# Kernel tuning notes

Hardware: AMD Instinct MI355X
Metric: run time of the kernel (lower is better)

The kernel has to match this reference:

```python
import jax, jax.numpy as jnp
import numpy as np

CLUSTER_DIM = 64
SHRINKAGE = True
EPS = 1e-8


def setup_inputs() -> dict:
    key = jax.random.key(0)
    x = jax.random.normal(key, (256, CLUSTER_DIM, 4096), dtype=jnp.float32)
    return {"x": x}


def _mat_shrinkage(C, n):
    # Rao-Blackwellized Ledoit-Wolf shrinkage toward scaled identity.
    p = CLUSTER_DIM
    I = jnp.eye(p, dtype=C.dtype)[None, :, :]
    trace = jnp.trace(C, axis1=-2, axis2=-1)[:, None, None]          # [B,1,1]
    F_hat = trace / p * I
    second_trace = jnp.einsum('bij,bji->b', C, C)[:, None, None]      # tr(C @ C)
    numerator = (n - 2) / n * second_trace + trace ** 2
    denominator = (n + 2) * (second_trace - trace ** 2 / p)
    rho = jnp.minimum(numerator / denominator, 1.0)
    return rho * F_hat + (1.0 - rho) * C


def reference(x):
    B, C, M = x.shape  # C == CLUSTER_DIM
    x_mu = jnp.mean(x, axis=2, keepdims=True)
    x_cnt = x - x_mu                                                  # [B,C,M]
    cov = jnp.einsum('bcm,bdm->bcd', x_cnt, x_cnt) / M                # [B,C,C]
    if SHRINKAGE:
        cov = _mat_shrinkage(cov, n=M)
    L, Q = jnp.linalg.eigh(cov)                                       # L:[B,C] Q:[B,C,C]
    L = jnp.maximum(L, EPS)
    # S_hat = Q @ diag(L^-1/2) @ Q^T, fused as scaled columns of Q
    S_hat = jnp.einsum('bik,bk,bjk->bij', Q, jax.lax.rsqrt(L), Q)     # [B,C,C]
    Z = jnp.einsum('bij,bjm->bim', S_hat, x_cnt)                      # [B,C,M]
    return Z
```

## Files before the change

kernel.cpp:

```cpp
#include <hip/hip_runtime.h>
#include <hip/hip_bf16.h>

#define BB 256
#define P 64
#define MM 4096
#define MC 128
#define MT 256

using bf16x8 = __attribute__((ext_vector_type(8))) short;
using f32x16 = __attribute__((ext_vector_type(16))) float;
using f32x4  = __attribute__((ext_vector_type(4))) float;
using u32x4  = __attribute__((ext_vector_type(4))) unsigned;
using u32x2  = __attribute__((ext_vector_type(2))) unsigned;

__device__ inline f32x16 MF(bf16x8 a, bf16x8 b, f32x16 c) {
    return __builtin_amdgcn_mfma_f32_32x32x16_bf16(a, b, c, 0, 0, 0);
}
__device__ inline unsigned cvtpk(float lo, float hi) {
    unsigned u;
    asm("v_cvt_pk_bf16_f32 %0, %1, %2" : "=v"(u) : "v"(lo), "v"(hi));
    return u;
}

template<bool XPK>
__global__ __launch_bounds__(256)
void covpart_kernel(const float* __restrict__ x, float* __restrict__ s2p,
                    float* __restrict__ s1p, unsigned* __restrict__ xpk, int nsplit)
{
    __shared__ __align__(16) unsigned char smem[34816];

    const int b = blockIdx.x, sp = blockIdx.y;
    const int t = threadIdx.x;
    const int w = t >> 6, l = t & 63;
    const int lr = l & 31, lh = l >> 5;
    const int mlen = MM / nsplit;
    const float* xb = x + (size_t)b * (P * MM) + (size_t)sp * mlen;
    unsigned* xpb = XPK ? (xpk + (size_t)b * (32 * MM) + (size_t)sp * mlen) : nullptr;

    f32x16 acc0 = {0,0,0,0,0,0,0,0,0,0,0,0,0,0,0,0};
    f32x16 acc1 = {0,0,0,0,0,0,0,0,0,0,0,0,0,0,0,0};
    f32x16 acc2 = {0,0,0,0,0,0,0,0,0,0,0,0,0,0,0,0};
    f32x16 accse = {0,0,0,0,0,0,0,0,0,0,0,0,0,0,0,0};
    f32x16 accso = {0,0,0,0,0,0,0,0,0,0,0,0,0,0,0,0};
    const bf16x8 ones = {0x3F80,0x3F80,0x3F80,0x3F80,0x3F80,0x3F80,0x3F80,0x3F80};

    const int kbase = lh * 16;
    const int nch = mlen / MC;

    f32x4 ve[4], vo[4];
    #pragma unroll
    for (int j = 0; j < 4; ++j) {
        int slot = t + 256 * j;
        int dp = slot >> 5, c = (slot & 31) << 2;
        const float* p = xb + (size_t)(2 * dp) * MM + c;
        ve[j] = *reinterpret_cast<const f32x4*>(p);
        vo[j] = *reinterpret_cast<const f32x4*>(p + MM);
    }

    for (int ch = 0; ch < nch; ++ch) {
        char* buf = (char*)smem + (ch & 1) * 17408;
        #pragma unroll
        for (int j = 0; j < 4; ++j) {
            int slot = t + 256 * j;
            int dp = slot >> 5, c4 = slot & 31;
            float e0 = ve[j].x, e1 = ve[j].y, e2 = ve[j].z, e3 = ve[j].w;
            float o0 = vo[j].x, o1 = vo[j].y, o2 = vo[j].z, o3 = vo[j].w;
            u32x2 he, ho;
            he.x = cvtpk(e0, e1); he.y = cvtpk(e2, e3);
            ho.x = cvtpk(o0, o1); ho.y = cvtpk(o2, o3);
            char* dst = buf + (2 * dp) * 272 + c4 * 8;
            *reinterpret_cast<u32x2*>(dst) = he;
            *reinterpret_cast<u32x2*>(dst + 272) = ho;
            if (XPK) {
                u32x4 pd;
                pd.x = cvtpk(e0, o0); pd.y = cvtpk(e1, o1);
                pd.z = cvtpk(e2, o2); pd.w = cvtpk(e3, o3);
                *reinterpret_cast<u32x4*>(xpb + (size_t)dp * MM + ch * MC + c4 * 4) = pd;
            }
        }
        if (ch + 1 < nch) {
            const int m0 = (ch + 1) * MC;
            #pragma unroll
            for (int j = 0; j < 4; ++j) {
                int slot = t + 256 * j;
                int dp = slot >> 5, c = (slot & 31) << 2;
                const float* p = xb + (size_t)(2 * dp) * MM + m0 + c;
                ve[j] = *reinterpret_cast<const f32x4*>(p);
                vo[j] = *reinterpret_cast<const f32x4*>(p + MM);
            }
        }
        __syncthreads();
        #pragma unroll
        for (int kk = 0; kk < 2; ++kk) {
            const int kb = (2 * w + kk) * 32 + kbase;
            bf16x8 f0 = *(const bf16x8*)(buf + lr * 272 + kb);
            bf16x8 f1 = *(const bf16x8*)(buf + (32 + lr) * 272 + kb);
            acc0 = MF(f0, f0, acc0);
            acc1 = MF(f0, f1, acc1);
            acc2 = MF(f1, f1, acc2);
            accse = MF(f0, ones, accse);
            accso = MF(f1, ones, accso);
        }
    }

    float (*T)[32][33] = reinterpret_cast<float (*)[32][33]>(smem);
    float* s2b = s2p + ((size_t)sp * BB + b) * (P * P);
    float* s1b = s1p + ((size_t)sp * BB + b) * P;

#define REDUCE_PASS(ACC, STORE)                                       \
    {                                                                 \
        __syncthreads();                                              \
        _Pragma("unroll")                                             \
        for (int n = 0; n < 16; ++n) {                                \
            int row = (n & 3) + 8 * (n >> 2) + 4 * lh;                \
            T[w][row][lr] = ACC[n];                                   \
        }                                                             \
        __syncthreads();                                              \
        _Pragma("unroll")                                             \
        for (int q = 0; q < 4; ++q) {                                 \
            int idx = t + 256 * q;                                    \
            int r = idx >> 5, c = idx & 31;                           \
            float s = T[0][r][c] + T[1][r][c] + T[2][r][c] + T[3][r][c]; \
            STORE                                                     \
        }                                                             \
    }

    REDUCE_PASS(acc0, s2b[r * 64 + c] = s;)
    REDUCE_PASS(acc1, s2b[r * 64 + 32 + c] = s; s2b[(32 + c) * 64 + r] = s;)
    REDUCE_PASS(acc2, s2b[(32 + r) * 64 + 32 + c] = s;)
    REDUCE_PASS(accse, if (c == 0) s1b[r] = s;)
    REDUCE_PASS(accso, if (c == 0) s1b[32 + r] = s;)
#undef REDUCE_PASS
}

typedef float (*Mat68)[68];

__device__ inline void mm64f(Mat68 D, Mat68 A, Mat68 Bm, int t, float alpha, float beta)
{
    __syncthreads();
    const int r0 = (t >> 4) * 4, c0 = (t & 15) * 4;
    float acc[4][4];
    #pragma unroll
    for (int i = 0; i < 4; ++i)
        #pragma unroll
        for (int j = 0; j < 4; ++j) acc[i][j] = 0.f;
    #pragma unroll 4
    for (int k = 0; k < P; ++k) {
        float av[4], bv[4];
        *reinterpret_cast<float4*>(av) = *reinterpret_cast<const float4*>(&A[k][r0]);
        *reinterpret_cast<float4*>(bv) = *reinterpret_cast<const float4*>(&Bm[k][c0]);
        #pragma unroll
        for (int i = 0; i < 4; ++i)
            #pragma unroll
            for (int j = 0; j < 4; ++j) acc[i][j] += av[i] * bv[j];
    }
    __syncthreads();
    #pragma unroll
    for (int i = 0; i < 4; ++i)
        #pragma unroll
        for (int j = 0; j < 4; ++j)
            D[r0 + i][c0 + j] = alpha * acc[i][j] + ((r0 + i) == (c0 + j) ? beta : 0.f);
}

__global__ __launch_bounds__(256)
void whiten_kernel(const float* __restrict__ s2p, const float* __restrict__ s1p,
                   unsigned* __restrict__ sbb, float* __restrict__ tvec, int nsplit)
{
    __shared__ __align__(16) float B0[P][68], B1[P][68], B2[P][68], B3[P][68], B4[P][68];
    __shared__ float mus[P];
    __shared__ float red[2][4];
    const int b = blockIdx.x, t = threadIdx.x;

    if (t < P) {
        float s = 0.f;
        for (int sp = 0; sp < nsplit; ++sp) s += s1p[((size_t)sp * BB + b) * P + t];
        mus[t] = s * (1.0f / MM);
    }
    __syncthreads();

    float tr_part = 0.f, s2_part = 0.f;
    #pragma unroll
    for (int j = 0; j < 16; ++j) {
        int f = t + 256 * j;
        int i = f >> 6, jc = f & 63;
        float sum = 0.f;
        for (int sp = 0; sp < nsplit; ++sp)
            sum += s2p[((size_t)sp * BB + b) * (P * P) + f];
        float v = sum * (1.0f / MM) - mus[i] * mus[jc];
        B0[i][jc] = v;
        s2_part += v * v;
        if (i == jc) tr_part += v;
    }
    #pragma unroll
    for (int off = 32; off > 0; off >>= 1) {
        tr_part += __shfl_down(tr_part, off);
        s2_part += __shfl_down(s2_part, off);
    }
    if ((t & 63) == 0) { red[0][t >> 6] = tr_part; red[1][t >> 6] = s2_part; }
    __syncthreads();
    const float trace = red[0][0] + red[0][1] + red[0][2] + red[0][3];
    const float sum2  = red[1][0] + red[1][1] + red[1][2] + red[1][3];

    const float nf = (float)MM;
    const float num = (nf - 2.0f) / nf * sum2 + trace * trace;
    const float den = (nf + 2.0f) * (sum2 - trace * trace / (float)P);
    const float rho = (den > 0.f) ? fminf(num / den, 1.0f) : 1.0f;
    const float lam = trace * (1.0f / P);
    const float inv_s = 1.0f / lam;

    #pragma unroll
    for (int j = 0; j < 16; ++j) {
        int f = t + 256 * j;
        int i = f >> 6, jc = f & 63;
        float v = B0[i][jc];
        float sv = ((1.0f - rho) * v + ((i == jc) ? rho * lam : 0.f)) * inv_s;
        B0[i][jc] = sv;
        B2[i][jc] = ((i == jc) ? 1.5f : 0.f) - 0.5f * sv;
    }

    mm64f(B1, B0, B2, t, 1.f, 0.f);
    Mat68 Yc = B1, Zc = B2, Tc = B0, U = B3, V = B4;
    {
        mm64f(Tc, Zc, Yc, t, -0.5f, 1.5f);
        mm64f(U,  Yc, Tc, t, 1.f, 0.f);
        mm64f(V,  Tc, Zc, t, 1.f, 0.f);
        Mat68 tmp = Yc; Yc = U; U = tmp;
        tmp = Zc; Zc = V; V = tmp;
    }
    mm64f(Tc, Zc, Yc, t, -0.5f, 1.5f);
    mm64f(U,  Tc, Zc, t, 1.f, 0.f);
    __syncthreads();

    const float sc = rsqrtf(lam);
    unsigned* sb = sbb + (size_t)b * (P * P / 2);
    #pragma unroll
    for (int j = 0; j < 8; ++j) {
        int slot = t + 256 * j;
        int dp = slot >> 6, row = slot & 63;
        sb[slot] = cvtpk(U[row][2 * dp] * sc, U[row][2 * dp + 1] * sc);
    }
    if (t < P) {
        float tv = 0.f;
        #pragma unroll
        for (int d = 0; d < P; ++d) tv += U[t][d] * mus[d];
        tvec[b * P + t] = tv * sc;
    }
}

__global__ __launch_bounds__(256)
void apply_kernel_x(const unsigned* __restrict__ xpk, const unsigned* __restrict__ sbb,
                    const float* __restrict__ tvec, float* __restrict__ out)
{
    __shared__ unsigned Spk[32][68];
    __shared__ unsigned Xpk[32][260];
    __shared__ float tvs[P];
    const int mt = blockIdx.x, b = blockIdx.y;
    const int t = threadIdx.x;
    const int w = t >> 6, l = t & 63;
    const int lr = l & 31, lh = l >> 5;

    const unsigned* sb = sbb + (size_t)b * (P * P / 2);
    #pragma unroll
    for (int j = 0; j < 8; ++j) {
        int slot = t + 256 * j;
        Spk[slot >> 6][slot & 63] = sb[slot];
    }
    if (t < P) tvs[t] = tvec[b * P + t];

    const unsigned* xb = xpk + (size_t)b * (32 * MM) + mt * MT;
    #pragma unroll
    for (int j = 0; j < 8; ++j) {
        int slot = t + 256 * j;
        int dp = slot >> 6, m0 = (slot & 63) * 4;
        u32x4 pk = *reinterpret_cast<const u32x4*>(xb + (size_t)dp * MM + m0);
        *reinterpret_cast<u32x4*>(&Xpk[dp][m0]) = pk;
    }
    __syncthreads();

    union U8 { unsigned u[4]; bf16x8 v; };
    bf16x8 sa0[4], sa1[4];
    #pragma unroll
    for (int ks = 0; ks < 4; ++ks) {
        const int dpb = ks * 8 + lh * 4;
        U8 x0, x1;
        #pragma unroll
        for (int q = 0; q < 4; ++q) {
            x0.u[q] = Spk[dpb + q][lr];
            x1.u[q] = Spk[dpb + q][32 + lr];
        }
        sa0[ks] = x0.v;
        sa1[ks] = x1.v;
    }

    f32x16 acc00 = {0,0,0,0,0,0,0,0,0,0,0,0,0,0,0,0};
    f32x16 acc01 = {0,0,0,0,0,0,0,0,0,0,0,0,0,0,0,0};
    f32x16 acc10 = {0,0,0,0,0,0,0,0,0,0,0,0,0,0,0,0};
    f32x16 acc11 = {0,0,0,0,0,0,0,0,0,0,0,0,0,0,0,0};

    const int cq0 = (2 * w) * 32 + lr, cq1 = cq0 + 32;
    #pragma unroll
    for (int ks = 0; ks < 4; ++ks) {
        const int dpb = ks * 8 + lh * 4;
        U8 b0, b1;
        #pragma unroll
        for (int q = 0; q < 4; ++q) {
            b0.u[q] = Xpk[dpb + q][cq0];
            b1.u[q] = Xpk[dpb + q][cq1];
        }
        acc00 = MF(sa0[ks], b0.v, acc00);
        acc01 = MF(sa0[ks], b1.v, acc01);
        acc10 = MF(sa1[ks], b0.v, acc10);
        acc11 = MF(sa1[ks], b1.v, acc11);
    }

    float* ob = out + (size_t)b * (P * MM) + mt * MT;
#define STORE_TILE(ACC, RT, CQ)                                          \
    {                                                                    \
        _Pragma("unroll")                                                \
        for (int n = 0; n < 16; ++n) {                                   \
            int row = (RT) * 32 + (n & 3) + 8 * (n >> 2) + 4 * lh;       \
            __builtin_nontemporal_store(ACC[n] - tvs[row],               \
                                        ob + (size_t)row * MM + (CQ));   \
        }                                                                \
    }
    STORE_TILE(acc00, 0, cq0)
    STORE_TILE(acc01, 0, cq1)
    STORE_TILE(acc10, 1, cq0)
    STORE_TILE(acc11, 1, cq1)
#undef STORE_TILE
}

__global__ __launch_bounds__(256)
void apply_kernel(const float* __restrict__ x, const unsigned* __restrict__ sbb,
                  const float* __restrict__ tvec, float* __restrict__ out)
{
    __shared__ unsigned Spk[32][68];
    __shared__ unsigned Xpk[32][260];
    __shared__ float tvs[P];
    const int mt = blockIdx.x, b = blockIdx.y;
    const int t = threadIdx.x;
    const int w = t >> 6, l = t & 63;
    const int lr = l & 31, lh = l >> 5;

    const unsigned* sb = sbb + (size_t)b * (P * P / 2);
    #pragma unroll
    for (int j = 0; j < 8; ++j) {
        int slot = t + 256 * j;
        Spk[slot >> 6][slot & 63] = sb[slot];
    }
    if (t < P) tvs[t] = tvec[b * P + t];

    const float* xb = x + (size_t)b * (P * MM) + mt * MT;
    #pragma unroll
    for (int j = 0; j < 8; ++j) {
        int slot = t + 256 * j;
        int dp = slot >> 6, m0 = (slot & 63) * 4;
        const float* xr = xb + (size_t)(2 * dp) * MM + m0;
        f32x4 a = *reinterpret_cast<const f32x4*>(xr);
        f32x4 c = *reinterpret_cast<const f32x4*>(xr + MM);
        uint4 pk = make_uint4(cvtpk(a.x, c.x), cvtpk(a.y, c.y),
                              cvtpk(a.z, c.z), cvtpk(a.w, c.w));
        *reinterpret_cast<uint4*>(&Xpk[dp][m0]) = pk;
    }
    __syncthreads();

    union U8 { unsigned u[4]; bf16x8 v; };
    bf16x8 sa0[4], sa1[4];
    #pragma unroll
    for (int ks = 0; ks < 4; ++ks) {
        const int dpb = ks * 8 + lh * 4;
        U8 x0, x1;
        #pragma unroll
        for (int q = 0; q < 4; ++q) {
            x0.u[q] = Spk[dpb + q][lr];
            x1.u[q] = Spk[dpb + q][32 + lr];
        }
        sa0[ks] = x0.v;
        sa1[ks] = x1.v;
    }

    f32x16 acc00 = {0,0,0,0,0,0,0,0,0,0,0,0,0,0,0,0};
    f32x16 acc01 = {0,0,0,0,0,0,0,0,0,0,0,0,0,0,0,0};
    f32x16 acc10 = {0,0,0,0,0,0,0,0,0,0,0,0,0,0,0,0};
    f32x16 acc11 = {0,0,0,0,0,0,0,0,0,0,0,0,0,0,0,0};

    const int cq0 = (2 * w) * 32 + lr, cq1 = cq0 + 32;
    #pragma unroll
    for (int ks = 0; ks < 4; ++ks) {
        const int dpb = ks * 8 + lh * 4;
        U8 b0, b1;
        #pragma unroll
        for (int q = 0; q < 4; ++q) {
            b0.u[q] = Xpk[dpb + q][cq0];
            b1.u[q] = Xpk[dpb + q][cq1];
        }
        acc00 = MF(sa0[ks], b0.v, acc00);
        acc01 = MF(sa0[ks], b1.v, acc01);
        acc10 = MF(sa1[ks], b0.v, acc10);
        acc11 = MF(sa1[ks], b1.v, acc11);
    }

    float* ob = out + (size_t)b * (P * MM) + mt * MT;
#define STORE_TILE(ACC, RT, CQ)                                          \
    {                                                                    \
        _Pragma("unroll")                                                \
        for (int n = 0; n < 16; ++n) {                                   \
            int row = (RT) * 32 + (n & 3) + 8 * (n >> 2) + 4 * lh;       \
            __builtin_nontemporal_store(ACC[n] - tvs[row],               \
                                        ob + (size_t)row * MM + (CQ));   \
        }                                                                \
    }
    STORE_TILE(acc00, 0, cq0)
    STORE_TILE(acc01, 0, cq1)
    STORE_TILE(acc10, 1, cq0)
    STORE_TILE(acc11, 1, cq1)
#undef STORE_TILE
}

extern "C" void kernel_launch(void* const* d_in, const int* in_sizes, int n_in,
                              void* d_out, int out_size, void* d_ws, size_t ws_size,
                              hipStream_t stream)
{
    const float* x = (const float*)d_in[0];
    float* out = (float*)d_out;

    auto need = [](int ns) -> size_t {
        return ((size_t)ns * BB * P * P + (size_t)ns * BB * P
                + (size_t)BB * P * P / 2 + (size_t)BB * P) * sizeof(float);
    };
    const size_t xpk_bytes = (size_t)BB * 32 * MM * sizeof(unsigned);

    int nsplit;
    bool xon;
    if (ws_size >= need(4) + xpk_bytes)      { nsplit = 4; xon = true; }
    else if (ws_size >= need(2) + xpk_bytes) { nsplit = 2; xon = true; }
    else {
        xon = false;
        nsplit = (ws_size >= need(4)) ? 4 : (ws_size >= need(2)) ? 2 : 1;
    }

    float* s2p  = (float*)d_ws;
    float* s1p  = s2p + (size_t)nsplit * BB * P * P;
    unsigned* sbb = (unsigned*)(s1p + (size_t)nsplit * BB * P);
    float* tvec = (float*)(sbb + (size_t)BB * P * P / 2);
    unsigned* xpk = (unsigned*)(tvec + (size_t)BB * P);

    if (xon) {
        covpart_kernel<true><<<dim3(BB, nsplit), 256, 0, stream>>>(x, s2p, s1p, xpk, nsplit);
        whiten_kernel<<<dim3(BB), 256, 0, stream>>>(s2p, s1p, sbb, tvec, nsplit);
        apply_kernel_x<<<dim3(MM / MT, BB), 256, 0, stream>>>(xpk, sbb, tvec, out);
    } else {
        covpart_kernel<false><<<dim3(BB, nsplit), 256, 0, stream>>>(x, s2p, s1p, nullptr, nsplit);
        whiten_kernel<<<dim3(BB), 256, 0, stream>>>(s2p, s1p, sbb, tvec, nsplit);
        apply_kernel<<<dim3(MM / MT, BB), 256, 0, stream>>>(x, sbb, tvec, out);
    }
}
```

Baseline: 187.3 us.

## Split fp32-to-bf16 packing into a separate convert kernel before covariance

Adds a standalone convert kernel that reads fp32 x with nontemporal loads and writes the interleaved bf16 pair-packed buffer. The covariance kernel then reads the half-size packed buffer and unpacks it with bit ops instead of converting fp32 itself. The aim is to decouple the bandwidth-heavy conversion from the MFMA accumulation and give it more parallelism. The cost is an extra kernel launch and an extra read of the packed buffer.

Result: slower. 199.6 us (+6.6%).

```diff
diff --git a/kernel.cpp b/kernel.cpp
--- a/kernel.cpp
+++ b/kernel.cpp
@@ -22,10 +22,31 @@
     return u;
 }
 
-template<bool XPK>
 __global__ __launch_bounds__(256)
-void covpart_kernel(const float* __restrict__ x, float* __restrict__ s2p,
-                    float* __restrict__ s1p, unsigned* __restrict__ xpk, int nsplit)
+void convert_kernel(const float* __restrict__ x, unsigned* __restrict__ xpk)
+{
+    const int bp = blockIdx.x;
+    const int b = bp >> 3, sub = bp & 7;
+    const int t = threadIdx.x;
+    const float* xb = x + (size_t)b * (P * MM) + sub * 512;
+    unsigned* xpb = xpk + (size_t)b * (32 * MM) + sub * 512;
+    #pragma unroll
+    for (int j = 0; j < 16; ++j) {
+        int slot = t + 256 * j;
+        int dp = slot >> 7, c4 = slot & 127;
+        const float* p = xb + (size_t)(2 * dp) * MM + c4 * 4;
+        f32x4 e = __builtin_nontemporal_load(reinterpret_cast<const f32x4*>(p));
+        f32x4 o = __builtin_nontemporal_load(reinterpret_cast<const f32x4*>(p + MM));
+        u32x4 pd;
+        pd.x = cvtpk(e.x, o.x); pd.y = cvtpk(e.y, o.y);
+        pd.z = cvtpk(e.z, o.z); pd.w = cvtpk(e.w, o.w);
+        *reinterpret_cast<u32x4*>(xpb + (size_t)dp * MM + c4 * 4) = pd;
+    }
+}
+
+__global__ __launch_bounds__(256)
+void covpart2_kernel(const unsigned* __restrict__ xpk, float* __restrict__ s2p,
+                     float* __restrict__ s1p, int nsplit)
 {
     __shared__ __align__(16) unsigned char smem[34816];
 
@@ -34,8 +55,7 @@
     const int w = t >> 6, l = t & 63;
     const int lr = l & 31, lh = l >> 5;
     const int mlen = MM / nsplit;
-    const float* xb = x + (size_t)b * (P * MM) + (size_t)sp * mlen;
-    unsigned* xpb = XPK ? (xpk + (size_t)b * (32 * MM) + (size_t)sp * mlen) : nullptr;
+    const unsigned* xpb = xpk + (size_t)b * (32 * MM) + (size_t)sp * mlen;
 
     f32x16 acc0 = {0,0,0,0,0,0,0,0,0,0,0,0,0,0,0,0};
     f32x16 acc1 = {0,0,0,0,0,0,0,0,0,0,0,0,0,0,0,0};
@@ -47,14 +67,12 @@
     const int kbase = lh * 16;
     const int nch = mlen / MC;
 
-    f32x4 ve[4], vo[4];
+    u32x4 v[4];
     #pragma unroll
     for (int j = 0; j < 4; ++j) {
         int slot = t + 256 * j;
-        int dp = slot >> 5, c = (slot & 31) << 2;
-        const float* p = xb + (size_t)(2 * dp) * MM + c;
-        ve[j] = *reinterpret_cast<const f32x4*>(p);
-        vo[j] = *reinterpret_cast<const f32x4*>(p + MM);
+        int dp = slot >> 5, c4 = slot & 31;
+        v[j] = *reinterpret_cast<const u32x4*>(xpb + (size_t)dp * MM + c4 * 4);
     }
 
     for (int ch = 0; ch < nch; ++ch) {
@@ -63,30 +81,23 @@
         for (int j = 0; j < 4; ++j) {
             int slot = t + 256 * j;
             int dp = slot >> 5, c4 = slot & 31;
-            float e0 = ve[j].x, e1 = ve[j].y, e2 = ve[j].z, e3 = ve[j].w;
-            float o0 = vo[j].x, o1 = vo[j].y, o2 = vo[j].z, o3 = vo[j].w;
+            unsigned d0 = v[j].x, d1 = v[j].y, d2 = v[j].z, d3 = v[j].w;
             u32x2 he, ho;
-            he.x = cvtpk(e0, e1); he.y = cvtpk(e2, e3);
-            ho.x = cvtpk(o0, o1); ho.y = cvtpk(o2, o3);
+            he.x = (d0 & 0xFFFFu) | (d1 << 16);
+            he.y = (d2 & 0xFFFFu) | (d3 << 16);
+            ho.x = (d0 >> 16) | (d1 & 0xFFFF0000u);
+            ho.y = (d2 >> 16) | (d3 & 0xFFFF0000u);
             char* dst = buf + (2 * dp) * 272 + c4 * 8;
             *reinterpret_cast<u32x2*>(dst) = he;
             *reinterpret_cast<u32x2*>(dst + 272) = ho;
-            if (XPK) {
-                u32x4 pd;
-                pd.x = cvtpk(e0, o0); pd.y = cvtpk(e1, o1);
-                pd.z = cvtpk(e2, o2); pd.w = cvtpk(e3, o3);
-                *reinterpret_cast<u32x4*>(xpb + (size_t)dp * MM + ch * MC + c4 * 4) = pd;
-            }
         }
         if (ch + 1 < nch) {
             const int m0 = (ch + 1) * MC;
             #pragma unroll
             for (int j = 0; j < 4; ++j) {
                 int slot = t + 256 * j;
-                int dp = slot >> 5, c = (slot & 31) << 2;
-                const float* p = xb + (size_t)(2 * dp) * MM + m0 + c;
-                ve[j] = *reinterpret_cast<const f32x4*>(p);
-                vo[j] = *reinterpret_cast<const f32x4*>(p + MM);
+                int dp = slot >> 5, c4 = slot & 31;
+                v[j] = *reinterpret_cast<const u32x4*>(xpb + (size_t)dp * MM + m0 + c4 * 4);
             }
         }
         __syncthreads();
@@ -133,6 +144,107 @@
 #undef REDUCE_PASS
 }
 
+__global__ __launch_bounds__(256)
+void covpart_kernel(const float* __restrict__ x, float* __restrict__ s2p,
+                    float* __restrict__ s1p, int nsplit)
+{
+    __shared__ __align__(16) unsigned char smem[34816];
+
+    const int b = blockIdx.x, sp = blockIdx.y;
+    const int t = threadIdx.x;
+    const int w = t >> 6, l = t & 63;
+    const int lr = l & 31, lh = l >> 5;
+    const int mlen = MM / nsplit;
+    const float* xb = x + (size_t)b * (P * MM) + (size_t)sp * mlen;
+
+    f32x16 acc0 = {0,0,0,0,0,0,0,0,0,0,0,0,0,0,0,0};
+    f32x16 acc1 = {0,0,0,0,0,0,0,0,0,0,0,0,0,0,0,0};
+    f32x16 acc2 = {0,0,0,0,0,0,0,0,0,0,0,0,0,0,0,0};
+    f32x16 accse = {0,0,0,0,0,0,0,0,0,0,0,0,0,0,0,0};
+    f32x16 accso = {0,0,0,0,0,0,0,0,0,0,0,0,0,0,0,0};
+    const bf16x8 ones = {0x3F80,0x3F80,0x3F80,0x3F80,0x3F80,0x3F80,0x3F80,0x3F80};
+
+    const int kbase = lh * 16;
+    const int nch = mlen / MC;
+
+    f32x4 ve[4], vo[4];
+    #pragma unroll
+    for (int j = 0; j < 4; ++j) {
+        int slot = t + 256 * j;
+        int dp = slot >> 5, c = (slot & 31) << 2;
+        const float* p = xb + (size_t)(2 * dp) * MM + c;
+        ve[j] = *reinterpret_cast<const f32x4*>(p);
+        vo[j] = *reinterpret_cast<const f32x4*>(p + MM);
+    }
+
+    for (int ch = 0; ch < nch; ++ch) {
+        char* buf = (char*)smem + (ch & 1) * 17408;
+        #pragma unroll
+        for (int j = 0; j < 4; ++j) {
+            int slot = t + 256 * j;
+            int dp = slot >> 5, c4 = slot & 31;
+            u32x2 he, ho;
+            he.x = cvtpk(ve[j].x, ve[j].y); he.y = cvtpk(ve[j].z, ve[j].w);
+            ho.x = cvtpk(vo[j].x, vo[j].y); ho.y = cvtpk(vo[j].z, vo[j].w);
+            char* dst = buf + (2 * dp) * 272 + c4 * 8;
+            *reinterpret_cast<u32x2*>(dst) = he;
+            *reinterpret_cast<u32x2*>(dst + 272) = ho;
+        }
+        if (ch + 1 < nch) {
+            const int m0 = (ch + 1) * MC;
+            #pragma unroll
+            for (int j = 0; j < 4; ++j) {
+                int slot = t + 256 * j;
+                int dp = slot >> 5, c = (slot & 31) << 2;
+                const float* p = xb + (size_t)(2 * dp) * MM + m0 + c;
+                ve[j] = *reinterpret_cast<const f32x4*>(p);
+                vo[j] = *reinterpret_cast<const f32x4*>(p + MM);
+            }
+        }
+        __syncthreads();
+        #pragma unroll
+        for (int kk = 0; kk < 2; ++kk) {
+            const int kb = (2 * w + kk) * 32 + kbase;
+            bf16x8 f0 = *(const bf16x8*)(buf + lr * 272 + kb);
+            bf16x8 f1 = *(const bf16x8*)(buf + (32 + lr) * 272 + kb);
+            acc0 = MF(f0, f0, acc0);
+            acc1 = MF(f0, f1, acc1);
+            acc2 = MF(f1, f1, acc2);
+            accse = MF(f0, ones, accse);
+            accso = MF(f1, ones, accso);
+        }
+    }
+
+    float (*T)[32][33] = reinterpret_cast<float (*)[32][33]>(smem);
+    float* s2b = s2p + ((size_t)sp * BB + b) * (P * P);
+    float* s1b = s1p + ((size_t)sp * BB + b) * P;
+
+#define REDUCE_PASS(ACC, STORE)                                       \
+    {                                                                 \
+        __syncthreads();                                              \
+        _Pragma("unroll")                                             \
+        for (int n = 0; n < 16; ++n) {                                \
+            int row = (n & 3) + 8 * (n >> 2) + 4 * lh;                \
+            T[w][row][lr] = ACC[n];                                   \
+        }                                                             \
+        __syncthreads();                                              \
+        _Pragma("unroll")                                             \
+        for (int q = 0; q < 4; ++q) {                                 \
+            int idx = t + 256 * q;                                    \
+            int r = idx >> 5, c = idx & 31;                           \
+            float s = T[0][r][c] + T[1][r][c] + T[2][r][c] + T[3][r][c]; \
+            STORE                                                     \
+        }                                                             \
+    }
+
+    REDUCE_PASS(acc0, s2b[r * 64 + c] = s;)
+    REDUCE_PASS(acc1, s2b[r * 64 + 32 + c] = s; s2b[(32 + c) * 64 + r] = s;)
+    REDUCE_PASS(acc2, s2b[(32 + r) * 64 + 32 + c] = s;)
+    REDUCE_PASS(accse, if (c == 0) s1b[r] = s;)
+    REDUCE_PASS(accso, if (c == 0) s1b[32 + r] = s;)
+#undef REDUCE_PASS
+}
+
 typedef float (*Mat68)[68];
 
 __device__ inline void mm64f(Mat68 D, Mat68 A, Mat68 Bm, int t, float alpha, float beta)
@@ -446,11 +558,12 @@
     unsigned* xpk = (unsigned*)(tvec + (size_t)BB * P);
 
     if (xon) {
-        covpart_kernel<true><<<dim3(BB, nsplit), 256, 0, stream>>>(x, s2p, s1p, xpk, nsplit);
+        convert_kernel<<<dim3(BB * 8), 256, 0, stream>>>(x, xpk);
+        covpart2_kernel<<<dim3(BB, nsplit), 256, 0, stream>>>(xpk, s2p, s1p, nsplit);
         whiten_kernel<<<dim3(BB), 256, 0, stream>>>(s2p, s1p, sbb, tvec, nsplit);
         apply_kernel_x<<<dim3(MM / MT, BB), 256, 0, stream>>>(xpk, sbb, tvec, out);
     } else {
-        covpart_kernel<false><<<dim3(BB, nsplit), 256, 0, stream>>>(x, s2p, s1p, nullptr, nsplit);
+        covpart_kernel<<<dim3(BB, nsplit), 256, 0, stream>>>(x, s2p, s1p, nsplit);
         whiten_kernel<<<dim3(BB), 256, 0, stream>>>(s2p, s1p, sbb, tvec, nsplit);
         apply_kernel<<<dim3(MM / MT, BB), 256, 0, stream>>>(x, sbb, tvec, out);
     }
```
